# Optimization experiments

Hardware: AMD Instinct MI355X
Metric: run time of the kernel (lower is better)

## Reference

```python
import jax, jax.numpy as jnp
import numpy as np

B, S, DIM_VAL, DIM_ATTN = 8, 2048, 512, 512

def setup_inputs() -> dict:
    key = jax.random.key(0)
    k1, k2, k3, k4 = jax.random.split(key, 4)
    x = jax.random.normal(k1, (B, S, DIM_VAL), dtype=jnp.float32)
    # nn.Linear weights are [out_features, in_features], no bias
    scale = 1.0 / np.sqrt(DIM_VAL)
    Wq = jax.random.uniform(k2, (DIM_ATTN, DIM_VAL), dtype=jnp.float32, minval=-scale, maxval=scale)
    Wk = jax.random.uniform(k3, (DIM_ATTN, DIM_VAL), dtype=jnp.float32, minval=-scale, maxval=scale)
    Wv = jax.random.uniform(k4, (DIM_VAL, DIM_VAL), dtype=jnp.float32, minval=-scale, maxval=scale)
    return {"x": x, "Wq": Wq, "Wk": Wk, "Wv": Wv}

def reference(x, Wq, Wk, Wv):
    # Q,K: [B,S,dim_attn]; V: [B,S,dim_val]
    Q = jnp.einsum('bsd,ad->bsa', x, Wq)
    K = jnp.einsum('bsd,ad->bsa', x, Wk)
    V = jnp.einsum('bsd,vd->bsv', x, Wv)
    scores = jnp.einsum('bqa,bka->bqk', Q, K) / jnp.sqrt(jnp.asarray(Q.shape[-1], dtype=Q.dtype))
    attn = jax.nn.softmax(scores, axis=-1)
    return jnp.einsum('bqk,bkv->bqv', attn, V)
```

## Files before the change

kernel.cpp:

```cpp
#include <hip/hip_runtime.h>
#include <hip/hip_bf16.h>
#include <math.h>

#define BQ   8
#define SEQ  2048
#define DV   512
#define DA   512
#define MTOT (BQ * SEQ)

typedef __attribute__((ext_vector_type(8))) short bf16x8;
typedef __attribute__((ext_vector_type(4))) float f32x4;
typedef __attribute__((ext_vector_type(4))) short short4v;

__device__ __forceinline__ unsigned short f2bf(float f) {
    union { float f; unsigned u; } c; c.f = f;
    unsigned u = c.u;
    unsigned r = (u + 0x7fffu + ((u >> 16) & 1u)) >> 16;
    return (unsigned short)r;
}
__device__ __forceinline__ float bf2f(unsigned short h) {
    union { unsigned u; float f; } c; c.u = ((unsigned)h) << 16;
    return c.f;
}

__device__ __forceinline__ void gload_lds16(const void* g, void* l) {
    __builtin_amdgcn_global_load_lds(
        (const __attribute__((address_space(1))) void*)g,
        (__attribute__((address_space(3))) void*)l,
        16, 0, 0);
}

__global__ __launch_bounds__(256) void cvt_f32_bf16(
    const float* __restrict__ in, short* __restrict__ out, int n4)
{
    int i = blockIdx.x * blockDim.x + threadIdx.x;
    int stride = gridDim.x * blockDim.x;
    for (; i < n4; i += stride) {
        float4 v = ((const float4*)in)[i];
        short4v o;
        o[0] = (short)f2bf(v.x);
        o[1] = (short)f2bf(v.y);
        o[2] = (short)f2bf(v.z);
        o[3] = (short)f2bf(v.w);
        ((short4v*)out)[i] = o;
    }
}

template<int OMODE>
__global__ __launch_bounds__(256, 2) void gemm_bt(
    const short* __restrict__ A, const short* __restrict__ B, void* __restrict__ Cv,
    int M, int N, int K, int lda, int ldb, int ldc,
    long strideA, long strideB, long strideC, float scale)
{
    __shared__ __align__(16) short sA[128 * 32];
    __shared__ __align__(16) short sB[128 * 32];

    const int tid  = threadIdx.x;
    const int wave = tid >> 6;
    const int lane = tid & 63;
    const int wr = wave >> 1, wc = wave & 1;
    const int brow = blockIdx.y * 128;
    const int bcol = blockIdx.x * 128;
    const int z = blockIdx.z;
    A += (size_t)z * strideA;
    B += (size_t)z * strideB;

    const int r16 = lane & 15;
    const int kq  = lane >> 4;
    const int csw = (kq ^ (r16 & 3)) * 8;

    f32x4 acc[4][4];
    const f32x4 fz = {0.f, 0.f, 0.f, 0.f};
    #pragma unroll
    for (int i = 0; i < 4; ++i)
        #pragma unroll
        for (int j = 0; j < 4; ++j) acc[i][j] = fz;

    for (int k0 = 0; k0 < K; k0 += 32) {
        #pragma unroll
        for (int j = 0; j < 2; ++j) {
            int slot = wave * 128 + j * 64 + lane;
            int row  = slot >> 2;
            int cs   = (slot & 3) ^ (row & 3);
            const short* ga = A + (size_t)(brow + row) * lda + k0 + cs * 8;
            const short* gb = B + (size_t)(bcol + row) * ldb + k0 + cs * 8;
            int ldsoff = (wave * 128 + j * 64) * 8;
            gload_lds16(ga, &sA[ldsoff]);
            gload_lds16(gb, &sB[ldsoff]);
        }
        __syncthreads();

        bf16x8 a[4], b[4];
        #pragma unroll
        for (int i = 0; i < 4; ++i)
            a[i] = *(const bf16x8*)&sA[(wr * 64 + i * 16 + r16) * 32 + csw];
        #pragma unroll
        for (int j = 0; j < 4; ++j)
            b[j] = *(const bf16x8*)&sB[(wc * 64 + j * 16 + r16) * 32 + csw];

        #pragma unroll
        for (int i = 0; i < 4; ++i)
            #pragma unroll
            for (int j = 0; j < 4; ++j)
                acc[i][j] = __builtin_amdgcn_mfma_f32_16x16x32_bf16(a[i], b[j], acc[i][j], 0, 0, 0);
        __syncthreads();
    }

    #pragma unroll
    for (int i = 0; i < 4; ++i) {
        int row0 = brow + wr * 64 + i * 16 + (lane >> 4) * 4;
        #pragma unroll
        for (int j = 0; j < 4; ++j) {
            int col = bcol + wc * 64 + j * 16 + (lane & 15);
            f32x4 v = acc[i][j];
            #pragma unroll
            for (int t = 0; t < 4; ++t) {
                int row = row0 + t;
                if (OMODE == 0) {
                    ((short*)Cv)[(size_t)z * strideC + (size_t)row * ldc + col] =
                        (short)f2bf(v[t] * scale);
                } else if (OMODE == 1) {
                    ((float*)Cv)[(size_t)z * strideC + (size_t)row * ldc + col] = v[t];
                } else {
                    short* Qb = (short*)Cv;
                    short* Kb = Qb + (size_t)MTOT * DA;
                    short* VT = Kb + (size_t)MTOT * DA;
                    if (col < 512) {
                        Qb[(size_t)row * DA + col] = (short)f2bf(v[t] * scale);
                    } else if (col < 1024) {
                        Kb[(size_t)row * DA + (col - 512)] = (short)f2bf(v[t]);
                    } else {
                        int vcol = col - 1024;
                        int bb = row >> 11;
                        int ss = row & (SEQ - 1);
                        VT[((size_t)bb * DV + vcol) * SEQ + ss] = (short)f2bf(v[t]);
                    }
                }
            }
        }
    }
}

__global__ __launch_bounds__(256) void softmax_rows(short* __restrict__ S)
{
    int row  = blockIdx.x * 4 + (threadIdx.x >> 6);
    int lane = threadIdx.x & 63;
    size_t base = (size_t)row * SEQ;

    float v[32];
    #pragma unroll
    for (int c = 0; c < 4; ++c) {
        bf16x8 x = *(const bf16x8*)&S[base + c * 512 + lane * 8];
        #pragma unroll
        for (int e = 0; e < 8; ++e) v[c * 8 + e] = bf2f((unsigned short)x[e]);
    }
    float mx = -1e30f;
    #pragma unroll
    for (int i = 0; i < 32; ++i) mx = fmaxf(mx, v[i]);
    #pragma unroll
    for (int off = 32; off > 0; off >>= 1) mx = fmaxf(mx, __shfl_xor(mx, off));

    float sum = 0.f;
    #pragma unroll
    for (int i = 0; i < 32; ++i) { v[i] = __expf(v[i] - mx); sum += v[i]; }
    #pragma unroll
    for (int off = 32; off > 0; off >>= 1) sum += __shfl_xor(sum, off);
    float inv = 1.0f / sum;

    #pragma unroll
    for (int c = 0; c < 4; ++c) {
        bf16x8 x;
        #pragma unroll
        for (int e = 0; e < 8; ++e) x[e] = (short)f2bf(v[c * 8 + e] * inv);
        *(bf16x8*)&S[base + c * 512 + lane * 8] = x;
    }
}

extern "C" void kernel_launch(void* const* d_in, const int* in_sizes, int n_in,
                              void* d_out, int out_size, void* d_ws, size_t ws_size,
                              hipStream_t stream)
{
    const float* x  = (const float*)d_in[0];
    const float* Wq = (const float*)d_in[1];
    const float* Wk = (const float*)d_in[2];
    const float* Wv = (const float*)d_in[3];
    float* out = (float*)d_out;

    short* xb  = (short*)d_ws;
    short* wqb = xb  + (size_t)MTOT * DV;
    short* wkb = wqb + (size_t)DA * DV;
    short* wvb = wkb + (size_t)DA * DV;
    short* Qb  = wvb + (size_t)DV * DV;
    short* Kb  = Qb  + (size_t)MTOT * DA;
    short* VT  = Kb  + (size_t)MTOT * DA;
    short* Sc  = VT  + (size_t)MTOT * DV;

    const float qscale = 0.04419417382415922f;

    cvt_f32_bf16<<<8192, 256, 0, stream>>>(x,  xb,  (MTOT * DV) / 4);
    cvt_f32_bf16<<<256,  256, 0, stream>>>(Wq, wqb, (DA * DV) / 4);
    cvt_f32_bf16<<<256,  256, 0, stream>>>(Wk, wkb, (DA * DV) / 4);
    cvt_f32_bf16<<<256,  256, 0, stream>>>(Wv, wvb, (DV * DV) / 4);

    dim3 blk(256);

    gemm_bt<3><<<dim3(12, 128, 1), blk, 0, stream>>>(
        xb, wqb, Qb, MTOT, 1536, DV, DV, DV, 0, 0, 0, 0, qscale);

    gemm_bt<0><<<dim3(16, 16, BQ), blk, 0, stream>>>(
        Qb, Kb, Sc, SEQ, SEQ, DA, DA, DA, SEQ,
        (long)SEQ * DA, (long)SEQ * DA, (long)SEQ * SEQ, 1.0f);

    softmax_rows<<<(BQ * SEQ) / 4, 256, 0, stream>>>(Sc);

    gemm_bt<1><<<dim3(4, 16, BQ), blk, 0, stream>>>(
        Sc, VT, out, SEQ, DV, SEQ, SEQ, SEQ, DV,
        (long)SEQ * SEQ, (long)DV * SEQ, (long)SEQ * DV, 1.0f);
}
```

Measured before the change: 281.4 us.

## Fuse QK^T, softmax and PV into a single flash-attention kernel

Replaces the separate score GEMM, row softmax and PV GEMM with one online-softmax kernel. Each block handles 64 query rows and streams K and V^T tiles straight from global memory, with a cross-wave max/sum exchange in LDS. This removes the round trip of the bf16 score matrix through HBM and two kernel launches. The cost is only 256 blocks of 512 threads, K/V fragments read from global memory without LDS staging, two barriers per tile, and heavy register use from a 32-entry Q fragment array per thread.

```diff
diff --git a/kernel.cpp b/kernel.cpp
--- a/kernel.cpp
+++ b/kernel.cpp
@@ -17,10 +17,6 @@
     unsigned u = c.u;
     unsigned r = (u + 0x7fffu + ((u >> 16) & 1u)) >> 16;
     return (unsigned short)r;
-}
-__device__ __forceinline__ float bf2f(unsigned short h) {
-    union { unsigned u; float f; } c; c.u = ((unsigned)h) << 16;
-    return c.f;
 }
 
 __device__ __forceinline__ void gload_lds16(const void* g, void* l) {
@@ -141,39 +137,197 @@
     }
 }
 
-__global__ __launch_bounds__(256) void softmax_rows(short* __restrict__ S)
+__global__ __launch_bounds__(512, 2) void flash_attn(
+    const short* __restrict__ Qb, const short* __restrict__ Kb,
+    const short* __restrict__ VT, float* __restrict__ out)
 {
-    int row  = blockIdx.x * 4 + (threadIdx.x >> 6);
-    int lane = threadIdx.x & 63;
-    size_t base = (size_t)row * SEQ;
-
-    float v[32];
-    #pragma unroll
-    for (int c = 0; c < 4; ++c) {
-        bf16x8 x = *(const bf16x8*)&S[base + c * 512 + lane * 8];
-        #pragma unroll
-        for (int e = 0; e < 8; ++e) v[c * 8 + e] = bf2f((unsigned short)x[e]);
-    }
-    float mx = -1e30f;
-    #pragma unroll
-    for (int i = 0; i < 32; ++i) mx = fmaxf(mx, v[i]);
-    #pragma unroll
-    for (int off = 32; off > 0; off >>= 1) mx = fmaxf(mx, __shfl_xor(mx, off));
-
-    float sum = 0.f;
-    #pragma unroll
-    for (int i = 0; i < 32; ++i) { v[i] = __expf(v[i] - mx); sum += v[i]; }
-    #pragma unroll
-    for (int off = 32; off > 0; off >>= 1) sum += __shfl_xor(sum, off);
-    float inv = 1.0f / sum;
-
-    #pragma unroll
-    for (int c = 0; c < 4; ++c) {
-        bf16x8 x;
-        #pragma unroll
-        for (int e = 0; e < 8; ++e) x[e] = (short)f2bf(v[c * 8 + e] * inv);
-        *(bf16x8*)&S[base + c * 512 + lane * 8] = x;
-    }
+    __shared__ __align__(16) short Pbuf[2][2][32 * 64];
+    __shared__ __align__(16) float mbuf[2][2][4][32];
+    __shared__ __align__(16) float sbuf[2][2][4][32];
+
+    const int tid  = threadIdx.x;
+    const int lane = tid & 63;
+    const int wv   = tid >> 6;
+    const int rg   = wv >> 2;
+    const int gd   = wv & 3;
+    const int r16  = lane & 15;
+    const int g4   = lane >> 4;
+
+    const int blk = blockIdx.x;
+    const int b   = blk >> 5;
+    const int qt  = blk & 31;
+    const int qrow0 = b * SEQ + qt * 64 + rg * 32;
+
+    const short* Kbase = Kb + (size_t)b * SEQ * DA;
+    const short* Vbase = VT + (size_t)b * DV * SEQ;
+
+    bf16x8 qf[2][16];
+    #pragma unroll
+    for (int rb = 0; rb < 2; ++rb)
+        #pragma unroll
+        for (int kc = 0; kc < 16; ++kc)
+            qf[rb][kc] = *(const bf16x8*)&Qb[(size_t)(qrow0 + rb * 16 + r16) * DA + kc * 32 + g4 * 8];
+
+    f32x4 of[2][8];
+    const f32x4 fz = {0.f, 0.f, 0.f, 0.f};
+    #pragma unroll
+    for (int rb = 0; rb < 2; ++rb)
+        #pragma unroll
+        for (int cb = 0; cb < 8; ++cb) of[rb][cb] = fz;
+
+    f32x4 m_run[2], l_run[2];
+    #pragma unroll
+    for (int rb = 0; rb < 2; ++rb) {
+        m_run[rb] = f32x4{-1e30f, -1e30f, -1e30f, -1e30f};
+        l_run[rb] = fz;
+    }
+
+    for (int t = 0; t < SEQ / 64; ++t) {
+        const int p  = t & 1;
+        const int k0 = t * 64;
+
+        f32x4 s[2] = {fz, fz};
+        #pragma unroll
+        for (int kc = 0; kc < 16; ++kc) {
+            bf16x8 kf = *(const bf16x8*)&Kbase[(size_t)(k0 + gd * 16 + r16) * DA + kc * 32 + g4 * 8];
+            s[0] = __builtin_amdgcn_mfma_f32_16x16x32_bf16(qf[0][kc], kf, s[0], 0, 0, 0);
+            s[1] = __builtin_amdgcn_mfma_f32_16x16x32_bf16(qf[1][kc], kf, s[1], 0, 0, 0);
+        }
+
+        f32x4 mt[2];
+        #pragma unroll
+        for (int rb = 0; rb < 2; ++rb) {
+            f32x4 v = s[rb];
+            #pragma unroll
+            for (int off = 1; off < 16; off <<= 1) {
+                v[0] = fmaxf(v[0], __shfl_xor(v[0], off));
+                v[1] = fmaxf(v[1], __shfl_xor(v[1], off));
+                v[2] = fmaxf(v[2], __shfl_xor(v[2], off));
+                v[3] = fmaxf(v[3], __shfl_xor(v[3], off));
+            }
+            mt[rb] = v;
+        }
+        if (r16 == 0) {
+            #pragma unroll
+            for (int rb = 0; rb < 2; ++rb)
+                *(f32x4*)&mbuf[p][rg][gd][rb * 16 + g4 * 4] = mt[rb];
+        }
+        __syncthreads();
+
+        f32x4 mnew[2], ps[2];
+        #pragma unroll
+        for (int rb = 0; rb < 2; ++rb) {
+            f32x4 mm = *(const f32x4*)&mbuf[p][rg][0][rb * 16 + g4 * 4];
+            #pragma unroll
+            for (int w = 1; w < 4; ++w) {
+                f32x4 o = *(const f32x4*)&mbuf[p][rg][w][rb * 16 + g4 * 4];
+                mm[0] = fmaxf(mm[0], o[0]); mm[1] = fmaxf(mm[1], o[1]);
+                mm[2] = fmaxf(mm[2], o[2]); mm[3] = fmaxf(mm[3], o[3]);
+            }
+            f32x4 mn;
+            mn[0] = fmaxf(m_run[rb][0], mm[0]); mn[1] = fmaxf(m_run[rb][1], mm[1]);
+            mn[2] = fmaxf(m_run[rb][2], mm[2]); mn[3] = fmaxf(m_run[rb][3], mm[3]);
+            mnew[rb] = mn;
+
+            f32x4 e;
+            e[0] = __expf(s[rb][0] - mn[0]); e[1] = __expf(s[rb][1] - mn[1]);
+            e[2] = __expf(s[rb][2] - mn[2]); e[3] = __expf(s[rb][3] - mn[3]);
+            s[rb] = e;
+
+            f32x4 v = e;
+            #pragma unroll
+            for (int off = 1; off < 16; off <<= 1) {
+                v[0] += __shfl_xor(v[0], off);
+                v[1] += __shfl_xor(v[1], off);
+                v[2] += __shfl_xor(v[2], off);
+                v[3] += __shfl_xor(v[3], off);
+            }
+            ps[rb] = v;
+
+            #pragma unroll
+            for (int c = 0; c < 4; ++c) {
+                int row = rb * 16 + g4 * 4 + c;
+                int col = gd * 16 + r16;
+                Pbuf[p][rg][row * 64 + (col ^ ((row & 7) * 8))] = (short)f2bf(e[c]);
+            }
+        }
+        if (r16 == 0) {
+            #pragma unroll
+            for (int rb = 0; rb < 2; ++rb)
+                *(f32x4*)&sbuf[p][rg][gd][rb * 16 + g4 * 4] = ps[rb];
+        }
+        __syncthreads();
+
+        bool up = false;
+        f32x4 scl[2];
+        #pragma unroll
+        for (int rb = 0; rb < 2; ++rb) {
+            f32x4 pt = *(const f32x4*)&sbuf[p][rg][0][rb * 16 + g4 * 4];
+            #pragma unroll
+            for (int w = 1; w < 4; ++w) {
+                f32x4 o = *(const f32x4*)&sbuf[p][rg][w][rb * 16 + g4 * 4];
+                pt[0] += o[0]; pt[1] += o[1]; pt[2] += o[2]; pt[3] += o[3];
+            }
+            f32x4 sc;
+            sc[0] = __expf(m_run[rb][0] - mnew[rb][0]);
+            sc[1] = __expf(m_run[rb][1] - mnew[rb][1]);
+            sc[2] = __expf(m_run[rb][2] - mnew[rb][2]);
+            sc[3] = __expf(m_run[rb][3] - mnew[rb][3]);
+            scl[rb] = sc;
+            up = up || sc[0] < 1.f || sc[1] < 1.f || sc[2] < 1.f || sc[3] < 1.f;
+            l_run[rb][0] = l_run[rb][0] * sc[0] + pt[0];
+            l_run[rb][1] = l_run[rb][1] * sc[1] + pt[1];
+            l_run[rb][2] = l_run[rb][2] * sc[2] + pt[2];
+            l_run[rb][3] = l_run[rb][3] * sc[3] + pt[3];
+            m_run[rb] = mnew[rb];
+        }
+        if (__any(up)) {
+            #pragma unroll
+            for (int rb = 0; rb < 2; ++rb)
+                #pragma unroll
+                for (int cb = 0; cb < 8; ++cb) {
+                    of[rb][cb][0] *= scl[rb][0];
+                    of[rb][cb][1] *= scl[rb][1];
+                    of[rb][cb][2] *= scl[rb][2];
+                    of[rb][cb][3] *= scl[rb][3];
+                }
+        }
+
+        #pragma unroll
+        for (int kc2 = 0; kc2 < 2; ++kc2) {
+            bf16x8 af[2];
+            #pragma unroll
+            for (int rb = 0; rb < 2; ++rb) {
+                int row = rb * 16 + r16;
+                int soff = row * 64 + ((kc2 * 32 + g4 * 8) ^ ((row & 7) * 8));
+                af[rb] = *(const bf16x8*)&Pbuf[p][rg][soff];
+            }
+            #pragma unroll
+            for (int cb = 0; cb < 8; ++cb) {
+                bf16x8 vf = *(const bf16x8*)&Vbase[
+                    (size_t)(gd * 128 + cb * 16 + r16) * SEQ + k0 + kc2 * 32 + g4 * 8];
+                of[0][cb] = __builtin_amdgcn_mfma_f32_16x16x32_bf16(af[0], vf, of[0][cb], 0, 0, 0);
+                of[1][cb] = __builtin_amdgcn_mfma_f32_16x16x32_bf16(af[1], vf, of[1][cb], 0, 0, 0);
+            }
+        }
+    }
+
+    f32x4 inv[2];
+    #pragma unroll
+    for (int rb = 0; rb < 2; ++rb) {
+        inv[rb][0] = 1.f / l_run[rb][0]; inv[rb][1] = 1.f / l_run[rb][1];
+        inv[rb][2] = 1.f / l_run[rb][2]; inv[rb][3] = 1.f / l_run[rb][3];
+    }
+    #pragma unroll
+    for (int rb = 0; rb < 2; ++rb)
+        #pragma unroll
+        for (int cb = 0; cb < 8; ++cb)
+            #pragma unroll
+            for (int c = 0; c < 4; ++c) {
+                int row  = qrow0 + rb * 16 + g4 * 4 + c;
+                int dcol = gd * 128 + cb * 16 + r16;
+                out[(size_t)row * DV + dcol] = of[rb][cb][c] * inv[rb][c];
+            }
 }
 
 extern "C" void kernel_launch(void* const* d_in, const int* in_sizes, int n_in,
@@ -193,7 +347,6 @@
     short* Qb  = wvb + (size_t)DV * DV;
     short* Kb  = Qb  + (size_t)MTOT * DA;
     short* VT  = Kb  + (size_t)MTOT * DA;
-    short* Sc  = VT  + (size_t)MTOT * DV;
 
     const float qscale = 0.04419417382415922f;
 
@@ -207,13 +360,5 @@
     gemm_bt<3><<<dim3(12, 128, 1), blk, 0, stream>>>(
         xb, wqb, Qb, MTOT, 1536, DV, DV, DV, 0, 0, 0, 0, qscale);
 
-    gemm_bt<0><<<dim3(16, 16, BQ), blk, 0, stream>>>(
-        Qb, Kb, Sc, SEQ, SEQ, DA, DA, DA, SEQ,
-        (long)SEQ * DA, (long)SEQ * DA, (long)SEQ * SEQ, 1.0f);
-
-    softmax_rows<<<(BQ * SEQ) / 4, 256, 0, stream>>>(Sc);
-
-    gemm_bt<1><<<dim3(4, 16, BQ), blk, 0, stream>>>(
-        Sc, VT, out, SEQ, DV, SEQ, SEQ, SEQ, DV,
-        (long)SEQ * SEQ, (long)DV * SEQ, (long)SEQ * DV, 1.0f);
-}
+    flash_attn<<<dim3(256, 1, 1), 512, 0, stream>>>(Qb, Kb, VT, out);
+}
```

After: 633.7 us. +125.1%, slower.
